# Performance work log

Hardware: AMD Instinct MI355X
Metric: run time of the kernel (lower is better)

## Reference

```python
import jax, jax.numpy as jnp
import numpy as np

B, R, A, S, SR = 128, 1024, 512, 196, 64


def _linear(x, w, b):
    return x @ w.T + b


def _lstm_cell(x, h, c, wih, whh, bih, bhh):
    # torch.nn.LSTMCell gate order: i, f, g, o
    g = x @ wih.T + bih + h @ whh.T + bhh
    i, f, gg, o = jnp.split(g, 4, axis=-1)
    c2 = jax.nn.sigmoid(f) * c + jax.nn.sigmoid(i) * jnp.tanh(gg)
    h2 = jax.nn.sigmoid(o) * jnp.tanh(c2)
    return h2, c2


def _attention(h, att_feats, p_att, mask, h2att_w, h2att_b, aw, ab):
    att_h = _linear(h, h2att_w, h2att_b)[:, None, :]            # [B,1,A]
    dot = jnp.tanh(p_att + att_h)                               # [B,S,A]
    e = jnp.einsum('bsa,a->bs', dot, aw[0]) + ab[0]             # alpha_net
    w = jax.nn.softmax(e, axis=1)
    w = w * mask
    w = w / jnp.sum(w, axis=1, keepdims=True)
    return jnp.einsum('bs,bsd->bd', w, att_feats)


def setup_inputs() -> dict:
    key = jax.random.key(0)
    ks = iter(jax.random.split(key, 80))
    def rn(shape, scale=1.0):
        return jax.random.normal(next(ks), shape, dtype=jnp.float32) * scale
    w = 0.02  # weight init scale
    inp = {
        'xt': rn((B, R)), 'state_h': rn((2, B, R)), 'state_c': rn((2, B, R)),
        'fc_feats': rn((B, R)),
        'att_feats': rn((B, S, R)), 'obj_feats': rn((B, S, R)),
        'attr_feats': rn((B, S, R)), 'rela_feats': rn((B, SR, R)),
        'p_obj_feats': rn((B, S, A)), 'p_attr_feats': rn((B, S, A)),
        'p_rela_feats': rn((B, SR, A)),
        'att_masks': jnp.ones((B, S), jnp.float32),
        'rela_masks': jnp.ones((B, SR), jnp.float32),
        'att_wih': rn((4*R, 3*R), w), 'att_whh': rn((4*R, R), w),
        'att_bih': rn((4*R,), w), 'att_bhh': rn((4*R,), w),
        'lang_wih': rn((4*R, 4*R), w), 'lang_whh': rn((4*R, R), w),
        'lang_bih': rn((4*R,), w), 'lang_bhh': rn((4*R,), w),
        'xt2_w': rn((R, R), w), 'xt2_b': rn((R,), w),
        'h_att2_w': rn((R, R), w), 'h_att2_b': rn((R,), w),
        'r_i2h_w': rn((R, 4*R), w), 'r_i2h_b': rn((R,), w),
        'r_h2h_w': rn((R, R), w), 'r_h2h_b': rn((R,), w),
        'huu_w': rn((R, 3*R), w), 'huu_b': rn((R,), w),
        'obj_h2att_w': rn((A, R), w), 'obj_h2att_b': rn((A,), w),
        'obj_alpha_w': rn((1, A), w), 'obj_alpha_b': rn((1,), w),
        'attr_h2att_w': rn((A, R), w), 'attr_h2att_b': rn((A,), w),
        'attr_alpha_w': rn((1, A), w), 'attr_alpha_b': rn((1,), w),
        'rela_h2att_w': rn((A, R), w), 'rela_h2att_b': rn((A,), w),
        'rela_alpha_w': rn((1, A), w), 'rela_alpha_b': rn((1,), w),
        'fr_lin_w': rn((R, R), w), 'fr_lin_b': rn((R,), w),
        'fr_emb_w': rn((R, R), w), 'fr_emb_b': rn((R,), w),
        'ho_lin_w': rn((R, R), w), 'ho_lin_b': rn((R,), w),
        'ho_emb_w': rn((R, R), w), 'ho_emb_b': rn((R,), w),
        'ada_alpha_w': rn((1, R), w), 'ada_alpha_b': rn((1,), w),
        'cfe_w': rn((R, A), w), 'cfe_b': rn((R,), w),
    }
    return inp


def reference(xt, state_h, state_c, fc_feats, att_feats, obj_feats, attr_feats,
              rela_feats, p_obj_feats, p_attr_feats, p_rela_feats, att_masks,
              rela_masks, att_wih, att_whh, att_bih, att_bhh, lang_wih,
              lang_whh, lang_bih, lang_bhh, xt2_w, xt2_b, h_att2_w, h_att2_b,
              r_i2h_w, r_i2h_b, r_h2h_w, r_h2h_b, huu_w, huu_b, obj_h2att_w,
              obj_h2att_b, obj_alpha_w, obj_alpha_b, attr_h2att_w,
              attr_h2att_b, attr_alpha_w, attr_alpha_b, rela_h2att_w,
              rela_h2att_b, rela_alpha_w, rela_alpha_b, fr_lin_w, fr_lin_b,
              fr_emb_w, fr_emb_b, ho_lin_w, ho_lin_b, ho_emb_w, ho_emb_b,
              ada_alpha_w, ada_alpha_b, cfe_w, cfe_b):
    # eval mode: all dropouts are identity
    prev_h = state_h[1]
    att_in = jnp.concatenate([prev_h, fc_feats, xt], axis=1)            # [B,3R]
    h_att_raw, c_att = _lstm_cell(att_in, state_h[0], state_c[0],
                                  att_wih, att_whh, att_bih, att_bhh)
    h_att = _linear(xt, xt2_w, xt2_b) + _linear(h_att_raw, h_att2_w, h_att2_b)
    att_obj = _attention(h_att, obj_feats, p_obj_feats, att_masks,
                         obj_h2att_w, obj_h2att_b, obj_alpha_w, obj_alpha_b)
    att_attr = _attention(h_att, attr_feats, p_attr_feats, att_masks,
                          attr_h2att_w, attr_h2att_b, attr_alpha_w, attr_alpha_b)
    att_rela = _attention(h_att, rela_feats, p_rela_feats, rela_masks,
                          rela_h2att_w, rela_h2att_b, rela_alpha_w, rela_alpha_b)
    lang_in = jnp.concatenate([h_att, att_obj, att_attr, att_rela], axis=1)  # [B,4R]
    h_lang, c_lang = _lstm_cell(lang_in, state_h[1], state_c[1],
                                lang_wih, lang_whh, lang_bih, lang_bhh)
    tanh_mt = jnp.tanh(c_lang)
    n5 = _linear(lang_in, r_i2h_w, r_i2h_b) + _linear(state_h[1], r_h2h_w, r_h2h_b)
    st = jax.nn.sigmoid(n5) * tanh_mt                                    # [B,R]
    # AdaAtt_attention(h_lang, st, att_feats, p_obj_feats)
    cfe = _linear(p_obj_feats, cfe_w, cfe_b)                             # [B,S,R]
    fake_region = jax.nn.relu(_linear(st, fr_lin_w, fr_lin_b))           # [B,R]
    fr_embed = _linear(fake_region, fr_emb_w, fr_emb_b)
    ho = jnp.tanh(_linear(h_lang, ho_lin_w, ho_lin_b))
    ho_embed = _linear(ho, ho_emb_w, ho_emb_b)
    img_all = jnp.concatenate([fake_region[:, None, :], att_feats], axis=1)    # [B,S+1,R]
    img_all_embed = jnp.concatenate([fr_embed[:, None, :], cfe], axis=1)
    hA = jnp.tanh(img_all_embed + ho_embed[:, None, :])
    e = jnp.einsum('bsr,r->bs', hA, ada_alpha_w[0]) + ada_alpha_b[0]
    PI = jax.nn.softmax(e, axis=1)                                       # [B,S+1]
    visAtt = jnp.einsum('bs,bsd->bd', PI, img_all)
    beta = PI[:, -1:]
    c_t_hat = beta * fake_region + (1.0 - beta) * visAtt
    output = _linear(jnp.concatenate([h_att, h_lang, c_t_hat], axis=1), huu_w, huu_b)
    new_h = jnp.stack([h_att, h_lang])
    new_c = jnp.stack([c_att, c_lang])
    return output, new_h, new_c
```

## Files before the change

### kernel.cpp

```cpp
#include <hip/hip_runtime.h>
#include <cstddef>

#define B 128
#define R 1024

typedef __attribute__((ext_vector_type(8))) short short8;
typedef __attribute__((ext_vector_type(4))) float f32x4;

__device__ __forceinline__ float sigf(float x) { return 1.0f / (1.0f + __expf(-x)); }

__device__ __forceinline__ short f2bf(float f) {
    unsigned int u = __float_as_uint(f);
    u += 0x7fff + ((u >> 16) & 1);
    return (short)(u >> 16);
}

__device__ __forceinline__ short8 cvt8(float4 u, float4 v) {
    short8 r;
    r[0] = f2bf(u.x); r[1] = f2bf(u.y); r[2] = f2bf(u.z); r[3] = f2bf(u.w);
    r[4] = f2bf(v.x); r[5] = f2bf(v.y); r[6] = f2bf(v.z); r[7] = f2bf(v.w);
    return r;
}

struct GJob {
    const float* A1; const float* A2; const float* A3;
    const float* W1; const float* W2; const float* W3;
    float* C;
    int lda1, lda2, lda3;
    int ldw1, ldw2, ldw3;
    int K1, K12, Ktot;
    int ldc, Kchunk, nb;
};

__global__ __launch_bounds__(256) void gemm_sk_kernel(GJob j0, GJob j1, GJob j2, int njobs)
{
    GJob j = j0;
    int nbx = blockIdx.x;
    if (njobs > 1 && nbx >= j.nb) { nbx -= j.nb; j = j1; }
    if (njobs > 2 && nbx >= j.nb) { nbx -= j.nb; j = j2; }

    const int bn   = nbx * 64;
    const int kbeg = blockIdx.y * j.Kchunk;
    const int kend = kbeg + j.Kchunk;

    __shared__ short sA[128 * 40];
    __shared__ short sB[64 * 40];
    const int tid  = threadIdx.x;
    const int rA   = tid >> 1;
    const int kha  = (tid & 1) << 4;
    const int rB   = tid >> 2;
    const int khb  = (tid & 3) << 3;
    const int lane = tid & 63;
    const int wid  = tid >> 6;
    const int wm   = wid * 32;
    const int fr_  = lane & 15;
    const int kof  = (lane >> 4) * 8;

    f32x4 acc[2][4];
#pragma unroll
    for (int m = 0; m < 2; ++m)
#pragma unroll
        for (int n = 0; n < 4; ++n)
            acc[m][n] = (f32x4)0.0f;

    for (int k0 = kbeg; k0 < kend; k0 += 32) {
        int kgA = k0 + kha;
        const float* pa;
        if (kgA < j.K1)       pa = j.A1 + (size_t)rA * j.lda1 + kgA;
        else if (kgA < j.K12) pa = j.A2 + (size_t)rA * j.lda2 + (kgA - j.K1);
        else                  pa = j.A3 + (size_t)rA * j.lda3 + (kgA - j.K12);
        int kgB = k0 + khb;
        const float* pw;
        if (kgB < j.K1)       pw = j.W1 + (size_t)(bn + rB) * j.ldw1 + kgB;
        else if (kgB < j.K12) pw = j.W2 + (size_t)(bn + rB) * j.ldw2 + (kgB - j.K1);
        else                  pw = j.W3 + (size_t)(bn + rB) * j.ldw3 + (kgB - j.K12);

        float4 a0 = ((const float4*)pa)[0];
        float4 a1 = ((const float4*)pa)[1];
        float4 a2 = ((const float4*)pa)[2];
        float4 a3 = ((const float4*)pa)[3];
        float4 w0 = ((const float4*)pw)[0];
        float4 w1 = ((const float4*)pw)[1];
        __syncthreads();
        *(short8*)&sA[rA * 40 + kha]     = cvt8(a0, a1);
        *(short8*)&sA[rA * 40 + kha + 8] = cvt8(a2, a3);
        *(short8*)&sB[rB * 40 + khb]     = cvt8(w0, w1);
        __syncthreads();
        short8 af[2], bf[4];
#pragma unroll
        for (int m = 0; m < 2; ++m)
            af[m] = *(const short8*)&sA[(wm + m * 16 + fr_) * 40 + kof];
#pragma unroll
        for (int n = 0; n < 4; ++n)
            bf[n] = *(const short8*)&sB[(n * 16 + fr_) * 40 + kof];
#pragma unroll
        for (int m = 0; m < 2; ++m)
#pragma unroll
            for (int n = 0; n < 4; ++n)
                acc[m][n] = __builtin_amdgcn_mfma_f32_16x16x32_bf16(af[m], bf[n], acc[m][n], 0, 0, 0);
    }

#pragma unroll
    for (int m = 0; m < 2; ++m) {
        int row0 = wm + m * 16 + ((lane >> 4) << 2);
#pragma unroll
        for (int n = 0; n < 4; ++n) {
            int col = bn + n * 16 + fr_;
#pragma unroll
            for (int rg = 0; rg < 4; ++rg)
                atomicAdd(&j.C[(size_t)(row0 + rg) * j.ldc + col], acc[m][n][rg]);
        }
    }
}

__global__ __launch_bounds__(256) void prologue_kernel(
    float* __restrict__ ws, int nws, float* __restrict__ o, const float* __restrict__ bias,
    const float* __restrict__ ph, const float* __restrict__ fc, const float* __restrict__ xt,
    float* __restrict__ att_in,
    const float* __restrict__ P, const float* __restrict__ W,
    short* __restrict__ Pbf, short* __restrict__ Wbf, int ZB)
{
    int blk = blockIdx.x;
    int tid = threadIdx.x;
    if (blk < ZB) {
        int idx = blk * 256 + tid;
        if (idx < nws) ws[idx] = 0.0f;
        else if (idx < nws + 131072) { int i = idx - nws; o[i] = bias[i & 1023]; }
        return;
    }
    blk -= ZB;
    if (blk < 384) {
        int idx = blk * 256 + tid;
        int r = idx / 768, c4 = idx - r * 768;
        int col = c4 * 4;
        const float* src = (col < 1024) ? (ph + (size_t)r * 1024 + col)
                         : (col < 2048) ? (fc + (size_t)r * 1024 + col - 1024)
                                        : (xt + (size_t)r * 1024 + col - 2048);
        *(float4*)(att_in + (size_t)r * 3072 + col) = *(const float4*)src;
        return;
    }
    blk -= 384;
    int lane = tid & 63;
    int fr = lane & 15, kg = lane >> 4;
    if (blk < 6272) {
        int w = blk * 4 + (tid >> 6);
        int rt = w >> 4, ks = w & 15;
        const float* src = P + (size_t)(rt * 16 + fr) * 512 + ks * 32 + kg * 8;
        float4 u = ((const float4*)src)[0];
        float4 v = ((const float4*)src)[1];
        *(short8*)(Pbf + ((size_t)w * 64 + lane) * 8) = cvt8(u, v);
    } else {
        int w = (blk - 6272) * 4 + (tid >> 6);
        int ct = w >> 4, ks = w & 15;
        const float* src = W + (size_t)(ct * 16 + fr) * 512 + ks * 32 + kg * 8;
        float4 u = ((const float4*)src)[0];
        float4 v = ((const float4*)src)[1];
        *(short8*)(Wbf + ((size_t)w * 64 + lane) * 8) = cvt8(u, v);
    }
}

__global__ __launch_bounds__(256, 2) void cfe_v5_kernel(
    const short* __restrict__ Pbf, const short* __restrict__ Wbf,
    const float* __restrict__ cb, const float* __restrict__ hoe,
    const float* __restrict__ ho_b, const float* __restrict__ aw,
    float* __restrict__ e)
{
    int p = blockIdx.x;
    int x8 = p & 7, rest = p >> 3;
    int n8 = rest & 7, q = rest >> 3;
    int m = q * 8 + x8;
    if (m >= 196) return;
    const int bm = m * 128, bn = n8 * 128;

    const int tid  = threadIdx.x;
    const int lane = tid & 63;
    const int wid  = tid >> 6;
    const int wm   = (wid >> 1) * 64;
    const int wn   = (wid & 1) * 64;
    const int fr_  = lane & 15;

    const short* pA = Pbf + (size_t)(bm + wm) * 512 + lane * 8;
    const short* pB = Wbf + (size_t)(bn + wn) * 512 + lane * 8;

    f32x4 acc[4][4];
#pragma unroll
    for (int mi = 0; mi < 4; ++mi)
#pragma unroll
        for (int n = 0; n < 4; ++n)
            acc[mi][n] = (f32x4)0.0f;

    short8 a[2][4], b[2][4];
#pragma unroll
    for (int mi = 0; mi < 4; ++mi) {
        a[0][mi] = *(const short8*)(pA + (mi * 16) * 512);
        b[0][mi] = *(const short8*)(pB + (mi * 16) * 512);
    }
#pragma unroll
    for (int ks = 0; ks < 16; ++ks) {
        const int cur = ks & 1, nxt = cur ^ 1;
        if (ks < 15) {
#pragma unroll
            for (int mi = 0; mi < 4; ++mi) {
                a[nxt][mi] = *(const short8*)(pA + (mi * 16 + ks + 1) * 512);
                b[nxt][mi] = *(const short8*)(pB + (mi * 16 + ks + 1) * 512);
            }
        }
#pragma unroll
        for (int mi = 0; mi < 4; ++mi)
#pragma unroll
            for (int n = 0; n < 4; ++n)
                acc[mi][n] = __builtin_amdgcn_mfma_f32_16x16x32_bf16(a[cur][mi], b[cur][n], acc[mi][n], 0, 0, 0);
    }

    const int l4 = lane >> 4;
    const int rbase = bm + wm + (l4 << 2);
    const int b0 = rbase / 196;
    const int b1 = (rbase + 51) / 196;
    float cba[4], awa[4], hv0[4], hv1[4];
#pragma unroll
    for (int n = 0; n < 4; ++n) {
        int col = bn + wn + n * 16 + fr_;
        cba[n] = cb[col] + ho_b[col];
        awa[n] = aw[col];
        hv0[n] = hoe[(size_t)b0 * R + col];
        hv1[n] = hoe[(size_t)b1 * R + col];
    }
#pragma unroll
    for (int mi = 0; mi < 4; ++mi) {
#pragma unroll
        for (int rg = 0; rg < 4; ++rg) {
            int gr = rbase + mi * 16 + rg;
            int bb = gr / 196;
            bool second = (bb != b0);
            float part = 0.0f;
#pragma unroll
            for (int n = 0; n < 4; ++n) {
                float hv = second ? hv1[n] : hv0[n];
                part += tanhf(acc[mi][n][rg] + cba[n] + hv) * awa[n];
            }
            part += __shfl_xor(part, 1);
            part += __shfl_xor(part, 2);
            part += __shfl_xor(part, 4);
            part += __shfl_xor(part, 8);
            if (fr_ == 0)
                atomicAdd(&e[bb * 197 + 1 + (gr - bb * 196)], part);
        }
    }
}

__global__ __launch_bounds__(256) void cfe_fallback_kernel(
    const float* __restrict__ P, const float* __restrict__ Wf,
    const float* __restrict__ cb, const float* __restrict__ hoe,
    const float* __restrict__ ho_b, const float* __restrict__ aw,
    float* __restrict__ e)
{
    int p = blockIdx.x;
    int x8 = p & 7, rest = p >> 3;
    int n8 = rest & 7, q = rest >> 3;
    int m = q * 8 + x8;
    if (m >= 196) return;
    const int bm = m * 128, bn = n8 * 128;

    __shared__ short sA[128 * 72];
    __shared__ short sB[128 * 72];
    const int tid  = threadIdx.x;
    const int lane = tid & 63;
    const int wid  = tid >> 6;
    const int wm   = (wid >> 1) * 64;
    const int wn   = (wid & 1) * 64;
    const int fr_  = lane & 15;
    const int kof  = (lane >> 4) * 8;

    f32x4 acc[4][4];
#pragma unroll
    for (int mi = 0; mi < 4; ++mi)
#pragma unroll
        for (int n = 0; n < 4; ++n)
            acc[mi][n] = (f32x4)0.0f;

    for (int k0 = 0; k0 < 512; k0 += 64) {
        __syncthreads();
        int row = tid >> 1;
        int half = (tid & 1) * 32;
        const float* pa = P + (size_t)(bm + row) * 512 + k0 + half;
        const float* pw = Wf + (size_t)(bn + row) * 512 + k0 + half;
#pragma unroll
        for (int c = 0; c < 32; c += 8) {
            float4 u = *(const float4*)(pa + c);
            float4 v = *(const float4*)(pa + c + 4);
            *(short8*)&sA[row * 72 + half + c] = cvt8(u, v);
            float4 uw = *(const float4*)(pw + c);
            float4 vw = *(const float4*)(pw + c + 4);
            *(short8*)&sB[row * 72 + half + c] = cvt8(uw, vw);
        }
        __syncthreads();
#pragma unroll
        for (int ks = 0; ks < 64; ks += 32) {
            short8 af[4], bf[4];
#pragma unroll
            for (int mi = 0; mi < 4; ++mi)
                af[mi] = *(const short8*)&sA[(wm + mi * 16 + fr_) * 72 + ks + kof];
#pragma unroll
            for (int n = 0; n < 4; ++n)
                bf[n] = *(const short8*)&sB[(wn + n * 16 + fr_) * 72 + ks + kof];
#pragma unroll
            for (int mi = 0; mi < 4; ++mi)
#pragma unroll
                for (int n = 0; n < 4; ++n)
                    acc[mi][n] = __builtin_amdgcn_mfma_f32_16x16x32_bf16(af[mi], bf[n], acc[mi][n], 0, 0, 0);
        }
    }

    const int l4 = lane >> 4;
    const int rbase = bm + wm + (l4 << 2);
    const int b0 = rbase / 196;
    const int b1 = (rbase + 51) / 196;
    float cba[4], awa[4], hv0[4], hv1[4];
#pragma unroll
    for (int n = 0; n < 4; ++n) {
        int col = bn + wn + n * 16 + fr_;
        cba[n] = cb[col] + ho_b[col];
        awa[n] = aw[col];
        hv0[n] = hoe[(size_t)b0 * R + col];
        hv1[n] = hoe[(size_t)b1 * R + col];
    }
#pragma unroll
    for (int mi = 0; mi < 4; ++mi) {
#pragma unroll
        for (int rg = 0; rg < 4; ++rg) {
            int gr = rbase + mi * 16 + rg;
            int bb = gr / 196;
            bool second = (bb != b0);
            float part = 0.0f;
#pragma unroll
            for (int n = 0; n < 4; ++n) {
                float hv = second ? hv1[n] : hv0[n];
                part += tanhf(acc[mi][n][rg] + cba[n] + hv) * awa[n];
            }
            part += __shfl_xor(part, 1);
            part += __shfl_xor(part, 2);
            part += __shfl_xor(part, 4);
            part += __shfl_xor(part, 8);
            if (fr_ == 0)
                atomicAdd(&e[bb * 197 + 1 + (gr - bb * 196)], part);
        }
    }
}

__global__ __launch_bounds__(256) void lstm_kernel(
    float* __restrict__ g, const float* __restrict__ bih, const float* __restrict__ bhh,
    const float* __restrict__ cprev, float* __restrict__ h, float* __restrict__ c,
    const float* __restrict__ n5, const float* __restrict__ nb1,
    const float* __restrict__ nb2, float* __restrict__ st)
{
    int t = blockIdx.x * 256 + threadIdx.x;
    int b = t >> 8, d4 = (t & 255) * 4;
    float* gr = g + (size_t)b * 4096;
    float4 gi = *(float4*)(gr + d4);
    float4 gf = *(float4*)(gr + 1024 + d4);
    float4 gg = *(float4*)(gr + 2048 + d4);
    float4 go = *(float4*)(gr + 3072 + d4);
    float4 bi1 = *(const float4*)(bih + d4),        bh1 = *(const float4*)(bhh + d4);
    float4 bi2 = *(const float4*)(bih + 1024 + d4), bh2 = *(const float4*)(bhh + 1024 + d4);
    float4 bi3 = *(const float4*)(bih + 2048 + d4), bh3 = *(const float4*)(bhh + 2048 + d4);
    float4 bi4 = *(const float4*)(bih + 3072 + d4), bh4 = *(const float4*)(bhh + 3072 + d4);
    float4 cp = *(const float4*)(cprev + (size_t)b * 1024 + d4);
    float4 zero = {0.f, 0.f, 0.f, 0.f};
    *(float4*)(gr + d4) = zero; *(float4*)(gr + 1024 + d4) = zero;
    *(float4*)(gr + 2048 + d4) = zero; *(float4*)(gr + 3072 + d4) = zero;
    float4 cc, hh;
    float iv, fv, gv, ov, c2, tc;
    iv = sigf(gi.x + bi1.x + bh1.x); fv = sigf(gf.x + bi2.x + bh2.x);
    gv = tanhf(gg.x + bi3.x + bh3.x); ov = sigf(go.x + bi4.x + bh4.x);
    c2 = fv * cp.x + iv * gv; tc = tanhf(c2); cc.x = c2; hh.x = ov * tc;
    float tcx = tc;
    iv = sigf(gi.y + bi1.y + bh1.y); fv = sigf(gf.y + bi2.y + bh2.y);
    gv = tanhf(gg.y + bi3.y + bh3.y); ov = sigf(go.y + bi4.y + bh4.y);
    c2 = fv * cp.y + iv * gv; tc = tanhf(c2); cc.y = c2; hh.y = ov * tc;
    float tcy = tc;
    iv = sigf(gi.z + bi1.z + bh1.z); fv = sigf(gf.z + bi2.z + bh2.z);
    gv = tanhf(gg.z + bi3.z + bh3.z); ov = sigf(go.z + bi4.z + bh4.z);
    c2 = fv * cp.z + iv * gv; tc = tanhf(c2); cc.z = c2; hh.z = ov * tc;
    float tcz = tc;
    iv = sigf(gi.w + bi1.w + bh1.w); fv = sigf(gf.w + bi2.w + bh2.w);
    gv = tanhf(gg.w + bi3.w + bh3.w); ov = sigf(go.w + bi4.w + bh4.w);
    c2 = fv * cp.w + iv * gv; tc = tanhf(c2); cc.w = c2; hh.w = ov * tc;
    float tcw = tc;
    *(float4*)(c + (size_t)b * 1024 + d4) = cc;
    *(float4*)(h + (size_t)b * 1024 + d4) = hh;
    if (st) {
        float4 nv = *(const float4*)(n5 + (size_t)b * 1024 + d4);
        float4 n1 = *(const float4*)(nb1 + d4), n2 = *(const float4*)(nb2 + d4);
        float4 sv;
        sv.x = sigf(nv.x + n1.x + n2.x) * tcx;
        sv.y = sigf(nv.y + n1.y + n2.y) * tcy;
        sv.z = sigf(nv.z + n1.z + n2.z) * tcz;
        sv.w = sigf(nv.w + n1.w + n2.w) * tcw;
        *(float4*)(st + (size_t)b * 1024 + d4) = sv;
    }
}

__global__ __launch_bounds__(256) void hatt_epi_kernel(
    float* __restrict__ lang_in, const float* __restrict__ b1,
    const float* __restrict__ b2, float* __restrict__ h_att_out)
{
    int t = blockIdx.x * 256 + threadIdx.x;
    int r = t >> 8, c4 = (t & 255) * 4;
    float4 v = *(float4*)(lang_in + (size_t)r * 4096 + c4);
    float4 x1 = *(const float4*)(b1 + c4), x2 = *(const float4*)(b2 + c4);
    v.x += x1.x + x2.x; v.y += x1.y + x2.y; v.z += x1.z + x2.z; v.w += x1.w + x2.w;
    *(float4*)(lang_in + (size_t)r * 4096 + c4) = v;
    *(float4*)(h_att_out + (size_t)r * 1024 + c4) = v;
}

__global__ __launch_bounds__(256) void att_e3_kernel(
    const float* __restrict__ p0, const float* __restrict__ p1, const float* __restrict__ p2,
    const float* __restrict__ ah3,
    const float* __restrict__ b0, const float* __restrict__ b1, const float* __restrict__ b2,
    const float* __restrict__ aw0, const float* __restrict__ aw1, const float* __restrict__ aw2,
    float* __restrict__ e3)
{
    int wid = threadIdx.x >> 6, lane = threadIdx.x & 63;
    int idx = blockIdx.x * 4 + wid;
    const float* p; const float* bb; const float* aw; int S, loc, mod;
    if (idx < 25088)      { mod = 0; loc = idx;          p = p0; bb = b0; aw = aw0; S = 196; }
    else if (idx < 50176) { mod = 1; loc = idx - 25088;  p = p1; bb = b1; aw = aw1; S = 196; }
    else                  { mod = 2; loc = idx - 50176;  p = p2; bb = b2; aw = aw2; S = 64; }
    int b = loc / S;
    const float4* pr = (const float4*)(p + (size_t)loc * 512);
    const float4* ab = (const float4*)(ah3 + (size_t)mod * 65536 + (size_t)b * 512);
    const float4* bb4 = (const float4*)bb;
    const float4* aw4 = (const float4*)aw;
    float sum = 0.0f;
#pragma unroll
    for (int k = 0; k < 2; ++k) {
        int a = k * 64 + lane;
        float4 pv = pr[a], av = ab[a], bv = bb4[a], wv = aw4[a];
        sum += tanhf(pv.x + av.x + bv.x) * wv.x;
        sum += tanhf(pv.y + av.y + bv.y) * wv.y;
        sum += tanhf(pv.z + av.z + bv.z) * wv.z;
        sum += tanhf(pv.w + av.w + bv.w) * wv.w;
    }
#pragma unroll
    for (int off = 32; off; off >>= 1) sum += __shfl_down(sum, off);
    if (lane == 0) e3[idx] = sum;
}

__global__ __launch_bounds__(256) void softmax3_kernel(
    float* __restrict__ e3, const float* __restrict__ am, const float* __restrict__ rm)
{
    __shared__ float red[256];
    int mod = blockIdx.x >> 7, b = blockIdx.x & 127, tid = threadIdx.x;
    int S = (mod == 2) ? 64 : 196;
    float* e = e3 + ((mod == 0) ? 0 : (mod == 1) ? 25088 : 50176) + (size_t)b * S;
    const float* mask = ((mod == 2) ? rm : am) + (size_t)b * S;
    float v = (tid < S) ? e[tid] : -3.4e38f;
    red[tid] = v; __syncthreads();
    for (int s = 128; s; s >>= 1) { if (tid < s) red[tid] = fmaxf(red[tid], red[tid + s]); __syncthreads(); }
    float m = red[0]; __syncthreads();
    float p = (tid < S) ? __expf(v - m) : 0.0f;
    red[tid] = p; __syncthreads();
    for (int s = 128; s; s >>= 1) { if (tid < s) red[tid] += red[tid + s]; __syncthreads(); }
    float s1 = red[0]; __syncthreads();
    float w = (tid < S) ? (p / s1) * mask[tid] : 0.0f;
    red[tid] = w; __syncthreads();
    for (int s = 128; s; s >>= 1) { if (tid < s) red[tid] += red[tid + s]; __syncthreads(); }
    float s2 = red[0];
    if (tid < S) e[tid] = w / s2;
}

__global__ __launch_bounds__(256) void wsum3_kernel(
    const float* __restrict__ e3,
    const float* __restrict__ f0, const float* __restrict__ f1, const float* __restrict__ f2,
    float* __restrict__ lang_in)
{
    int mod = blockIdx.x >> 7;
    int idx = (blockIdx.x & 127) * 256 + threadIdx.x;
    int b = idx >> 8, d4 = idx & 255;
    int S = (mod == 2) ? 64 : 196;
    int Sq = (S + 3) >> 2;
    int s0 = blockIdx.y * Sq, s1 = min(S, s0 + Sq);
    const float4* f = (const float4*)(((mod == 0) ? f0 : (mod == 1) ? f1 : f2) + ((size_t)b * S) * R) + d4;
    const float* wb = e3 + ((mod == 0) ? 0 : (mod == 1) ? 25088 : 50176) + (size_t)b * S;
    float4 acc = {0.f, 0.f, 0.f, 0.f};
#pragma unroll 4
    for (int s = s0; s < s1; ++s) {
        float w = wb[s];
        float4 fv = f[(size_t)s * 256];
        acc.x = fmaf(w, fv.x, acc.x); acc.y = fmaf(w, fv.y, acc.y);
        acc.z = fmaf(w, fv.z, acc.z); acc.w = fmaf(w, fv.w, acc.w);
    }
    float* dst = lang_in + (size_t)b * 4096 + 1024 + mod * 1024 + d4 * 4;
    atomicAdd(dst + 0, acc.x); atomicAdd(dst + 1, acc.y);
    atomicAdd(dst + 2, acc.z); atomicAdd(dst + 3, acc.w);
}

__global__ __launch_bounds__(256) void relutanh_kernel(
    float* __restrict__ fr, const float* __restrict__ frb,
    float* __restrict__ ho, const float* __restrict__ hob,
    float* __restrict__ ct_acc)
{
    int idx = blockIdx.x * 256 + threadIdx.x;
    int c = idx & 1023;
    if (idx < 131072) { fr[idx] = fmaxf(fr[idx] + frb[c], 0.0f); ct_acc[idx] = 0.0f; }
    else { int i = idx - 131072; ho[i] = tanhf(ho[i] + hob[c]); }
}

__global__ __launch_bounds__(256) void softmax_ada_kernel(
    float* __restrict__ e,
    const float* __restrict__ fre, const float* __restrict__ frb,
    const float* __restrict__ hoe, const float* __restrict__ hob,
    const float* __restrict__ aw)
{
    __shared__ float red[256];
    int b = blockIdx.x, tid = threadIdx.x;
    float s = 0.0f;
#pragma unroll
    for (int k = 0; k < 4; ++k) {
        int r = k * 256 + tid;
        s += tanhf(fre[(size_t)b * R + r] + frb[r] + hoe[(size_t)b * R + r] + hob[r]) * aw[r];
    }
    red[tid] = s; __syncthreads();
    for (int t = 128; t; t >>= 1) { if (tid < t) red[tid] += red[tid + t]; __syncthreads(); }
    float e0 = red[0]; __syncthreads();
    float v = (tid == 0) ? e0 : ((tid < 197) ? e[(size_t)b * 197 + tid] : -3.4e38f);
    red[tid] = v; __syncthreads();
    for (int t = 128; t; t >>= 1) { if (tid < t) red[tid] = fmaxf(red[tid], red[tid + t]); __syncthreads(); }
    float m = red[0]; __syncthreads();
    float p = (tid < 197) ? __expf(v - m) : 0.0f;
    red[tid] = p; __syncthreads();
    for (int t = 128; t; t >>= 1) { if (tid < t) red[tid] += red[tid + t]; __syncthreads(); }
    float s1 = red[0];
    if (tid < 197) e[(size_t)b * 197 + tid] = p / s1;
}

__global__ __launch_bounds__(256) void ct_part_kernel(
    const float* __restrict__ PI, const float* __restrict__ attf,
    float* __restrict__ ct_acc)
{
    int b = blockIdx.x, d4 = threadIdx.x;
    int s0 = blockIdx.y * 14, s1 = min(196, s0 + 14);
    const float* pb = PI + b * 197;
    const float4* af = (const float4*)(attf + ((size_t)b * 196) * R) + d4;
    float4 acc = {0.f, 0.f, 0.f, 0.f};
#pragma unroll 2
    for (int s = s0; s < s1; ++s) {
        float w = pb[1 + s];
        float4 av = af[(size_t)s * 256];
        acc.x = fmaf(w, av.x, acc.x); acc.y = fmaf(w, av.y, acc.y);
        acc.z = fmaf(w, av.z, acc.z); acc.w = fmaf(w, av.w, acc.w);
    }
    float* dst = ct_acc + (size_t)b * 1024 + d4 * 4;
    atomicAdd(dst + 0, acc.x); atomicAdd(dst + 1, acc.y);
    atomicAdd(dst + 2, acc.z); atomicAdd(dst + 3, acc.w);
}

__global__ __launch_bounds__(256) void ct_fin_kernel(
    const float* __restrict__ PI, const float* __restrict__ fr,
    const float* __restrict__ ct_acc, float* __restrict__ ct)
{
    int idx = blockIdx.x * 256 + threadIdx.x;
    int b = idx >> 10;
    const float* pb = PI + b * 197;
    float f = fr[idx];
    float acc = pb[0] * f + ct_acc[idx];
    float beta = pb[196];
    ct[idx] = beta * f + (1.0f - beta) * acc;
}

extern "C" void kernel_launch(void* const* d_in, const int* in_sizes, int n_in,
                              void* d_out, int out_size, void* d_ws, size_t ws_size,
                              hipStream_t stream)
{
    const float* xt         = (const float*)d_in[0];
    const float* state_h    = (const float*)d_in[1];
    const float* state_c    = (const float*)d_in[2];
    const float* fc_feats   = (const float*)d_in[3];
    const float* att_feats  = (const float*)d_in[4];
    const float* obj_feats  = (const float*)d_in[5];
    const float* attr_feats = (const float*)d_in[6];
    const float* rela_feats = (const float*)d_in[7];
    const float* p_obj      = (const float*)d_in[8];
    const float* p_attr     = (const float*)d_in[9];
    const float* p_rela     = (const float*)d_in[10];
    const float* att_masks  = (const float*)d_in[11];
    const float* rela_masks = (const float*)d_in[12];
    const float* att_wih    = (const float*)d_in[13];
    const float* att_whh    = (const float*)d_in[14];
    const float* att_bih    = (const float*)d_in[15];
    const float* att_bhh    = (const float*)d_in[16];
    const float* lang_wih   = (const float*)d_in[17];
    const float* lang_whh   = (const float*)d_in[18];
    const float* lang_bih   = (const float*)d_in[19];
    const float* lang_bhh   = (const float*)d_in[20];
    const float* xt2_w      = (const float*)d_in[21];
    const float* xt2_b      = (const float*)d_in[22];
    const float* h_att2_w   = (const float*)d_in[23];
    const float* h_att2_b   = (const float*)d_in[24];
    const float* r_i2h_w    = (const float*)d_in[25];
    const float* r_i2h_b    = (const float*)d_in[26];
    const float* r_h2h_w    = (const float*)d_in[27];
    const float* r_h2h_b    = (const float*)d_in[28];
    const float* huu_w      = (const float*)d_in[29];
    const float* huu_b      = (const float*)d_in[30];
    const float* obj_h2att_w  = (const float*)d_in[31];
    const float* obj_h2att_b  = (const float*)d_in[32];
    const float* obj_alpha_w  = (const float*)d_in[33];
    const float* attr_h2att_w = (const float*)d_in[35];
    const float* attr_h2att_b = (const float*)d_in[36];
    const float* attr_alpha_w = (const float*)d_in[37];
    const float* rela_h2att_w = (const float*)d_in[39];
    const float* rela_h2att_b = (const float*)d_in[40];
    const float* rela_alpha_w = (const float*)d_in[41];
    const float* fr_lin_w   = (const float*)d_in[43];
    const float* fr_lin_b   = (const float*)d_in[44];
    const float* fr_emb_w   = (const float*)d_in[45];
    const float* fr_emb_b   = (const float*)d_in[46];
    const float* ho_lin_w   = (const float*)d_in[47];
    const float* ho_lin_b   = (const float*)d_in[48];
    const float* ho_emb_w   = (const float*)d_in[49];
    const float* ho_emb_b   = (const float*)d_in[50];
    const float* ada_w      = (const float*)d_in[51];
    const float* cfe_w      = (const float*)d_in[53];
    const float* cfe_b      = (const float*)d_in[54];

    float* out = (float*)d_out;
    float* wsf = (float*)d_ws;

    float* g        = wsf + 0;
    float* lang_in  = wsf + 524288;
    float* att_h3   = wsf + 1048576;
    float* n5       = wsf + 1245184;
    float* fr       = wsf + 1376256;
    float* fre      = wsf + 1507328;
    float* ho       = wsf + 1638400;
    float* hoe      = wsf + 1769472;
    float* e_ada    = wsf + 1900544;
    const int NATOM = 1926144;
    float* att_in    = wsf + 1926144;
    float* ct_acc    = att_in;
    float* h_att_raw = wsf + 2319360;
    float* e3        = wsf + 2450432;
    float* st        = wsf + 2527232;
    float* ct        = wsf + 2658304;
    short* Pbf       = (short*)(wsf + 2789376);
    short* Wbf       = Pbf + 12845056;
    const bool big = ws_size >= (size_t)2789376 * 4 + (size_t)13369344 * 2;

    float* h_att_out  = out + 131072;
    float* h_lang_out = out + 262144;
    float* c_att_out  = out + 393216;
    float* c_lang_out = out + 524288;

    const float* prev_h = state_h + 131072;

    GJob Z = {};
    auto mk = [&](const float* A1, int lda1, int K1, const float* W1, int ldw1,
                  float* C, int ldc, int N, int Ktot, int Kchunk) {
        GJob j = Z;
        j.A1 = A1; j.lda1 = lda1; j.K1 = K1; j.K12 = Ktot; j.Ktot = Ktot;
        j.W1 = W1; j.ldw1 = ldw1;
        j.C = C; j.ldc = ldc; j.Kchunk = Kchunk; j.nb = N / 64;
        return j;
    };

    {
        const int ZB = (NATOM + 131072) / 256;
        int grid = ZB + 384 + (big ? 6528 : 0);
        prologue_kernel<<<grid, 256, 0, stream>>>(wsf, NATOM, out, huu_b,
            prev_h, fc_feats, xt, att_in, p_obj, cfe_w, Pbf, Wbf, ZB);
    }

    {
        GJob j = mk(att_in, 3072, 3072, att_wih, 3072, g, 4096, 4096, 4096, 512);
        j.A2 = state_h; j.lda2 = 1024; j.W2 = att_whh; j.ldw2 = 1024; j.K12 = 4096;
        gemm_sk_kernel<<<dim3(64, 8), 256, 0, stream>>>(j, Z, Z, 1);
    }
    lstm_kernel<<<128, 256, 0, stream>>>(g, att_bih, att_bhh, state_c, h_att_raw, c_att_out,
                                         nullptr, nullptr, nullptr, nullptr);

    {
        GJob j = mk(xt, 1024, 1024, xt2_w, 1024, lang_in, 4096, 1024, 2048, 128);
        j.A2 = h_att_raw; j.lda2 = 1024; j.W2 = h_att2_w; j.ldw2 = 1024; j.K12 = 2048;
        gemm_sk_kernel<<<dim3(16, 16), 256, 0, stream>>>(j, Z, Z, 1);
    }
    hatt_epi_kernel<<<128, 256, 0, stream>>>(lang_in, xt2_b, h_att2_b, h_att_out);

    {
        GJob j0 = mk(lang_in, 4096, 1024, obj_h2att_w,  1024, att_h3 + 0,      512, 512, 1024, 64);
        GJob j1 = mk(lang_in, 4096, 1024, attr_h2att_w, 1024, att_h3 + 65536,  512, 512, 1024, 64);
        GJob j2 = mk(lang_in, 4096, 1024, rela_h2att_w, 1024, att_h3 + 131072, 512, 512, 1024, 64);
        gemm_sk_kernel<<<dim3(24, 16), 256, 0, stream>>>(j0, j1, j2, 3);
    }
    att_e3_kernel<<<14592, 256, 0, stream>>>(p_obj, p_attr, p_rela, att_h3,
        obj_h2att_b, attr_h2att_b, rela_h2att_b, obj_alpha_w, attr_alpha_w, rela_alpha_w, e3);
    softmax3_kernel<<<384, 256, 0, stream>>>(e3, att_masks, rela_masks);
    wsum3_kernel<<<dim3(384, 4), 256, 0, stream>>>(e3, obj_feats, attr_feats, rela_feats, lang_in);

    {
        GJob j0 = mk(lang_in, 4096, 4096, lang_wih, 4096, g, 4096, 4096, 5120, 640);
        j0.A2 = prev_h; j0.lda2 = 1024; j0.W2 = lang_whh; j0.ldw2 = 1024; j0.K12 = 5120;
        GJob j1 = mk(lang_in, 4096, 4096, r_i2h_w, 4096, n5, 1024, 1024, 5120, 640);
        j1.A2 = prev_h; j1.lda2 = 1024; j1.W2 = r_h2h_w; j1.ldw2 = 1024; j1.K12 = 5120;
        gemm_sk_kernel<<<dim3(80, 8), 256, 0, stream>>>(j0, j1, Z, 2);
    }
    lstm_kernel<<<128, 256, 0, stream>>>(g, lang_bih, lang_bhh, state_c + 131072,
                                         h_lang_out, c_lang_out, n5, r_i2h_b, r_h2h_b, st);

    {
        GJob j0 = mk(st, 1024, 1024, fr_lin_w, 1024, fr, 1024, 1024, 1024, 64);
        GJob j1 = mk(h_lang_out, 1024, 1024, ho_lin_w, 1024, ho, 1024, 1024, 1024, 64);
        gemm_sk_kernel<<<dim3(32, 16), 256, 0, stream>>>(j0, j1, Z, 2);
    }
    relutanh_kernel<<<1024, 256, 0, stream>>>(fr, fr_lin_b, ho, ho_lin_b, ct_acc);

    {
        GJob j0 = mk(fr, 1024, 1024, fr_emb_w, 1024, fre, 1024, 1024, 1024, 64);
        GJob j1 = mk(ho, 1024, 1024, ho_emb_w, 1024, hoe, 1024, 1024, 1024, 64);
        gemm_sk_kernel<<<dim3(32, 16), 256, 0, stream>>>(j0, j1, Z, 2);
    }
    if (big) {
        cfe_v5_kernel<<<1600, 256, 0, stream>>>(Pbf, Wbf, cfe_b, hoe, ho_emb_b, ada_w, e_ada);
    } else {
        cfe_fallback_kernel<<<1600, 256, 0, stream>>>(p_obj, cfe_w, cfe_b, hoe, ho_emb_b, ada_w, e_ada);
    }
    softmax_ada_kernel<<<128, 256, 0, stream>>>(e_ada, fre, fr_emb_b, hoe, ho_emb_b, ada_w);
    ct_part_kernel<<<dim3(128, 14), 256, 0, stream>>>(e_ada, att_feats, ct_acc);
    ct_fin_kernel<<<512, 256, 0, stream>>>(e_ada, fr, ct_acc, ct);

    {
        GJob j = mk(lang_in, 4096, 1024, huu_w, 3072, out, 1024, 1024, 3072, 192);
        j.A2 = h_lang_out; j.lda2 = 1024; j.W2 = huu_w + 1024; j.ldw2 = 3072; j.K12 = 2048;
        j.A3 = ct; j.lda3 = 1024; j.W3 = huu_w + 2048; j.ldw3 = 3072;
        gemm_sk_kernel<<<dim3(16, 16), 256, 0, stream>>>(j, Z, Z, 1);
    }

    (void)in_sizes; (void)n_in; (void)out_size; (void)ws_size;
}
```

Measured before the change: 413.6 us.

## Stage cfe GEMM operands through LDS with async global_load_lds double buffering

```diff
diff --git a/kernel.cpp b/kernel.cpp
--- a/kernel.cpp
+++ b/kernel.cpp
@@ -20,6 +20,12 @@
     r[0] = f2bf(u.x); r[1] = f2bf(u.y); r[2] = f2bf(u.z); r[3] = f2bf(u.w);
     r[4] = f2bf(v.x); r[5] = f2bf(v.y); r[6] = f2bf(v.z); r[7] = f2bf(v.w);
     return r;
+}
+
+__device__ __forceinline__ void gll16(const void* g, void* l) {
+    __builtin_amdgcn_global_load_lds(
+        (const __attribute__((address_space(1))) unsigned int*)g,
+        (__attribute__((address_space(3))) unsigned int*)l, 16, 0, 0);
 }
 
 struct GJob {
@@ -159,7 +165,7 @@
     }
 }
 
-__global__ __launch_bounds__(256, 2) void cfe_v5_kernel(
+__global__ __launch_bounds__(256) void cfe_v7_kernel(
     const short* __restrict__ Pbf, const short* __restrict__ Wbf,
     const float* __restrict__ cb, const float* __restrict__ hoe,
     const float* __restrict__ ho_b, const float* __restrict__ aw,
@@ -172,15 +178,32 @@
     if (m >= 196) return;
     const int bm = m * 128, bn = n8 * 128;
 
+    __shared__ short sA[2][8 * 512];
+    __shared__ short sB[2][8 * 512];
+
     const int tid  = threadIdx.x;
     const int lane = tid & 63;
     const int wid  = tid >> 6;
     const int wm   = (wid >> 1) * 64;
     const int wn   = (wid & 1) * 64;
     const int fr_  = lane & 15;
-
-    const short* pA = Pbf + (size_t)(bm + wm) * 512 + lane * 8;
-    const short* pB = Wbf + (size_t)(bn + wn) * 512 + lane * 8;
+    const int rtbA = bm >> 4;
+    const int rtbB = bn >> 4;
+
+    auto STAGE = [&](int buf, int ks) {
+#pragma unroll
+        for (int jj = 0; jj < 4; ++jj) {
+            int fid = wid * 4 + jj;
+            int rt  = fid & 7;
+            if (fid < 8) {
+                const short* src = Pbf + ((size_t)((rtbA + rt) * 16 + ks) * 64 + lane) * 8;
+                gll16(src, &sA[buf][rt * 512]);
+            } else {
+                const short* src = Wbf + ((size_t)((rtbB + rt) * 16 + ks) * 64 + lane) * 8;
+                gll16(src, &sB[buf][rt * 512]);
+            }
+        }
+    };
 
     f32x4 acc[4][4];
 #pragma unroll
@@ -189,27 +212,24 @@
         for (int n = 0; n < 4; ++n)
             acc[mi][n] = (f32x4)0.0f;
 
-    short8 a[2][4], b[2][4];
-#pragma unroll
-    for (int mi = 0; mi < 4; ++mi) {
-        a[0][mi] = *(const short8*)(pA + (mi * 16) * 512);
-        b[0][mi] = *(const short8*)(pB + (mi * 16) * 512);
-    }
-#pragma unroll
-    for (int ks = 0; ks < 16; ++ks) {
-        const int cur = ks & 1, nxt = cur ^ 1;
-        if (ks < 15) {
-#pragma unroll
-            for (int mi = 0; mi < 4; ++mi) {
-                a[nxt][mi] = *(const short8*)(pA + (mi * 16 + ks + 1) * 512);
-                b[nxt][mi] = *(const short8*)(pB + (mi * 16 + ks + 1) * 512);
-            }
-        }
+    STAGE(0, 0);
+    for (int r = 0; r < 16; ++r) {
+        const int buf = r & 1;
+        __syncthreads();
+        if (r < 15) STAGE(buf ^ 1, r + 1);
+        short8 af[4], bf8[4];
 #pragma unroll
         for (int mi = 0; mi < 4; ++mi)
+            af[mi] = *(const short8*)&sA[buf][((wm >> 4) + mi) * 512 + lane * 8];
+#pragma unroll
+        for (int n = 0; n < 4; ++n)
+            bf8[n] = *(const short8*)&sB[buf][((wn >> 4) + n) * 512 + lane * 8];
+#pragma unroll
+        for (int mi = 0; mi < 4; ++mi)
 #pragma unroll
             for (int n = 0; n < 4; ++n)
-                acc[mi][n] = __builtin_amdgcn_mfma_f32_16x16x32_bf16(a[cur][mi], b[cur][n], acc[mi][n], 0, 0, 0);
+                acc[mi][n] = __builtin_amdgcn_mfma_f32_16x16x32_bf16(af[mi], bf8[n], acc[mi][n], 0, 0, 0);
+        __syncthreads();
     }
 
     const int l4 = lane >> 4;
@@ -720,7 +740,7 @@
         gemm_sk_kernel<<<dim3(32, 16), 256, 0, stream>>>(j0, j1, Z, 2);
     }
     if (big) {
-        cfe_v5_kernel<<<1600, 256, 0, stream>>>(Pbf, Wbf, cfe_b, hoe, ho_emb_b, ada_w, e_ada);
+        cfe_v7_kernel<<<1600, 256, 0, stream>>>(Pbf, Wbf, cfe_b, hoe, ho_emb_b, ada_w, e_ada);
     } else {
         cfe_fallback_kernel<<<1600, 256, 0, stream>>>(p_obj, cfe_w, cfe_b, hoe, ho_emb_b, ada_w, e_ada);
     }
```

New measurement: 407.8 us. Within noise of the previous version (-1.4%).
